# Performance work log

Measured on AMD Instinct MI355X. Metric: run time of the kernel, lower is better.

## Reference

```python
import jax, jax.numpy as jnp
import numpy as np


def setup_inputs() -> dict:
    key = jax.random.key(0)
    k1, k2 = jax.random.split(key)
    B, C, H, W = 8, 32, 384, 384
    # probability-map-like predictions in [0, 1)
    pred = jax.random.uniform(k1, (B, C, H, W), dtype=jnp.float32)
    target = jax.random.randint(k2, (B, H, W), 0, C)  # int labels, all classes present w.h.p.
    return {"pred": pred, "target": target}


def reference(pred, target):
    """J-statistic loss (arXiv:1910.09783). reduction='none', weights=ones.

    Original computes, for each ci != ck:
      loss[b,ci,ck] = w[ci,ck] * log(0.5 + sum_hw pred[b,ci]*(phi[b,ci]-phi[b,ck])/2)
    where phi = one_hot(target)/n_i. The O(C^2) loop collapses to a single
    batched contraction S[b,i,k] = <pred[b,i], phi[b,k]> over spatial dims.
    """
    B, C, H, W = pred.shape
    t1h = jax.nn.one_hot(target, C, dtype=pred.dtype)          # (B,H,W,C)
    t1h = jnp.moveaxis(t1h, -1, 1)                             # (B,C,H,W)
    n_i = t1h.sum(axis=(-2, -1))[:, :, None, None]             # (B,C,1,1) class pixel counts
    phi = t1h / n_i                                            # normalized one-hot
    # S[b,i,k] = sum_hw pred[b,i]*phi[b,k]
    S = jnp.einsum('bihw,bkhw->bik', pred, phi)                # (B,C,C)
    diag = jnp.diagonal(S, axis1=1, axis2=2)                   # (B,C) = S[b,i,i]
    delta_sum = (diag[:, :, None] - S) * 0.5                   # sum_hw pred_i * (phi_i - phi_k)/2
    weights = jnp.ones((C, C), dtype=pred.dtype)
    loss = weights * jnp.log(0.5 + delta_sum)                  # (B,C,C)
    off_diag = 1.0 - jnp.eye(C, dtype=pred.dtype)              # skip ci == ck terms
    j = -(loss * off_diag).sum(axis=(-2, -1))                  # (B,)
    return j
```

## Files before the change

### kernel.cpp

```cpp
#include <hip/hip_runtime.h>


#define BB 8
#define CC 32
#define HW 147456
#define CHUNK_PX 1024
#define NCHUNK (HW / CHUNK_PX)
#define HIST_BPB 16
#define HIST_SEG (HW / HIST_BPB)

typedef __attribute__((ext_vector_type(8))) short short8;
typedef __attribute__((ext_vector_type(4))) float float4v;

__device__ __forceinline__ short bf16_rne(float f) {
    union { float f; unsigned u; } v; v.f = f;
    unsigned u = v.u;
    u += 0x7FFFu + ((u >> 16) & 1u);
    return (short)(u >> 16);
}

__global__ __launch_bounds__(256) void jloss_mfma(
    const float* __restrict__ pred,
    const int*   __restrict__ target,
    float*       __restrict__ T)
{
    const int tid  = threadIdx.x;
    const int w    = tid >> 6;
    const int l    = tid & 63;
    const int quad = l >> 4;
    const int m    = l & 15;
    const int blk  = blockIdx.x;
    const int b    = blk / NCHUNK;
    const int chunk= blk % NCHUNK;

    const long pb_wave = (long)chunk * CHUNK_PX + w * 256;
    const float* predb = pred + (long)b * CC * HW;
    const int*   tgtb  = target + (long)b * HW;

    float4v acc00 = {0,0,0,0}, acc01 = {0,0,0,0};
    float4v acc10 = {0,0,0,0}, acc11 = {0,0,0,0};
    const short one = (short)0x3F80;

    #pragma unroll
    for (int ks = 0; ks < 8; ++ks) {
        const long po = pb_wave + ks * 32 + quad * 8;
        const float* p0 = predb + (long)m * HW + po;
        const float* p1 = p0 + (long)16 * HW;
        const float4 a0l = *(const float4*)p0;
        const float4 a0h = *(const float4*)(p0 + 4);
        const float4 a1l = *(const float4*)p1;
        const float4 a1h = *(const float4*)(p1 + 4);
        const int4 t0 = *(const int4*)(tgtb + po);
        const int4 t1 = *(const int4*)(tgtb + po + 4);

        short8 A0, A1, B0, B1;
        A0[0]=bf16_rne(a0l.x); A0[1]=bf16_rne(a0l.y); A0[2]=bf16_rne(a0l.z); A0[3]=bf16_rne(a0l.w);
        A0[4]=bf16_rne(a0h.x); A0[5]=bf16_rne(a0h.y); A0[6]=bf16_rne(a0h.z); A0[7]=bf16_rne(a0h.w);
        A1[0]=bf16_rne(a1l.x); A1[1]=bf16_rne(a1l.y); A1[2]=bf16_rne(a1l.z); A1[3]=bf16_rne(a1l.w);
        A1[4]=bf16_rne(a1h.x); A1[5]=bf16_rne(a1h.y); A1[6]=bf16_rne(a1h.z); A1[7]=bf16_rne(a1h.w);
        B0[0]=(t0.x==m)?one:(short)0; B0[1]=(t0.y==m)?one:(short)0;
        B0[2]=(t0.z==m)?one:(short)0; B0[3]=(t0.w==m)?one:(short)0;
        B0[4]=(t1.x==m)?one:(short)0; B0[5]=(t1.y==m)?one:(short)0;
        B0[6]=(t1.z==m)?one:(short)0; B0[7]=(t1.w==m)?one:(short)0;
        const int m16 = m + 16;
        B1[0]=(t0.x==m16)?one:(short)0; B1[1]=(t0.y==m16)?one:(short)0;
        B1[2]=(t0.z==m16)?one:(short)0; B1[3]=(t0.w==m16)?one:(short)0;
        B1[4]=(t1.x==m16)?one:(short)0; B1[5]=(t1.y==m16)?one:(short)0;
        B1[6]=(t1.z==m16)?one:(short)0; B1[7]=(t1.w==m16)?one:(short)0;

        acc00 = __builtin_amdgcn_mfma_f32_16x16x32_bf16(A0, B0, acc00, 0, 0, 0);
        acc01 = __builtin_amdgcn_mfma_f32_16x16x32_bf16(A0, B1, acc01, 0, 0, 0);
        acc10 = __builtin_amdgcn_mfma_f32_16x16x32_bf16(A1, B0, acc10, 0, 0, 0);
        acc11 = __builtin_amdgcn_mfma_f32_16x16x32_bf16(A1, B1, acc11, 0, 0, 0);
    }

    __shared__ float red[4][CC][CC];
    #pragma unroll
    for (int r = 0; r < 4; ++r) {
        red[w][quad*4 + r     ][m     ] = acc00[r];
        red[w][quad*4 + r     ][m + 16] = acc01[r];
        red[w][quad*4 + r + 16][m     ] = acc10[r];
        red[w][quad*4 + r + 16][m + 16] = acc11[r];
    }
    __syncthreads();

    float* Tb = T + (long)b * CC * CC;
    const float* rp = &red[0][0][0];
    for (int j = tid; j < CC * CC; j += 256) {
        const float s = rp[j] + rp[1024 + j] + rp[2048 + j] + rp[3072 + j];
        atomicAdd(&Tb[j], s);
    }
}

__global__ __launch_bounds__(256) void jloss_cnt(
    const int* __restrict__ target,
    float*     __restrict__ cnt)
{
    const int tid = threadIdx.x;
    const int w = tid >> 6, l = tid & 63;
    const int blk = blockIdx.x;
    const int b   = blk / HIST_BPB;
    const int seg = blk % HIST_BPB;
    const int* tb = target + (long)b * HW + (long)seg * HIST_SEG + w * (HIST_SEG / 4);

    int c[CC];
    #pragma unroll
    for (int k = 0; k < CC; ++k) c[k] = 0;
    for (int it = 0; it < HIST_SEG / 4 / 64; ++it) {
        const int t = tb[it * 64 + l];
        #pragma unroll
        for (int k = 0; k < CC; ++k)
            c[k] += (int)__popcll(__ballot(t == k));
    }
    if (l == 0) {
        #pragma unroll
        for (int k = 0; k < CC; ++k)
            atomicAdd(&cnt[b * CC + k], (float)c[k]);
    }
}

__global__ __launch_bounds__(256) void jloss_final(
    const float* __restrict__ T,
    const float* __restrict__ cnt,
    float*       __restrict__ out)
{
    const int b   = blockIdx.x;
    const int tid = threadIdx.x;
    __shared__ float diag_s[CC];
    __shared__ float inv_n[CC];
    __shared__ float wsum[4];

    const float* Tb = T + (long)b * CC * CC;
    const float* cb = cnt + b * CC;

    if (tid < CC) {
        const float inv = 1.0f / cb[tid];
        inv_n[tid]  = inv;
        diag_s[tid] = Tb[tid * CC + tid] * inv;
    }
    __syncthreads();

    float sum = 0.0f;
    for (int idx = tid; idx < CC * CC; idx += 256) {
        const int i = idx >> 5;
        const int k = idx & 31;
        if (i != k) {
            const float S = Tb[idx] * inv_n[k];
            sum += logf(0.5f + 0.5f * (diag_s[i] - S));
        }
    }
    #pragma unroll
    for (int off = 32; off > 0; off >>= 1) sum += __shfl_down(sum, off, 64);
    if ((tid & 63) == 0) wsum[tid >> 6] = sum;
    __syncthreads();
    if (tid == 0) out[b] = -(wsum[0] + wsum[1] + wsum[2] + wsum[3]);
}

extern "C" void kernel_launch(void* const* d_in, const int* in_sizes, int n_in,
                              void* d_out, int out_size, void* d_ws, size_t ws_size,
                              hipStream_t stream) {
    const float* pred   = (const float*)d_in[0];
    const int*   target = (const int*)d_in[1];
    float* out = (float*)d_out;

    float* T   = (float*)d_ws;
    float* cnt = (float*)d_ws + BB * CC * CC;

    hipMemsetAsync(d_ws, 0, (BB * CC * CC + BB * CC) * sizeof(float), stream);

    jloss_cnt <<<BB * HIST_BPB, 256, 0, stream>>>(target, cnt);
    jloss_mfma<<<BB * NCHUNK,   256, 0, stream>>>(pred, target, T);
    jloss_final<<<BB, 256, 0, stream>>>(T, cnt, out);
}
```

Before: 268.4 us.

## Fuse class counting into MFMA kernel and cheapen bf16/one-hot packing

Removes the separate histogram kernel. Class pixel counts are now produced inside the MFMA kernel by multiplying a row of bf16 ones against the one-hot B operands, then reduced through shared memory and added atomically into the count buffer. The per-element round-to-nearest bf16 conversion is replaced by a byte-permute that packs two truncated bf16 values per instruction. One-hot operands are built two at a time as packed 32-bit words. It also adds a launch-bounds occupancy hint and limits unrolling to 2, trading VALU work and one kernel launch for two extra MFMAs per step and slightly less accurate (truncated) bf16 inputs.

```diff
diff --git a/kernel.cpp b/kernel.cpp
--- a/kernel.cpp
+++ b/kernel.cpp
@@ -6,23 +6,23 @@
 #define HW 147456
 #define CHUNK_PX 1024
 #define NCHUNK (HW / CHUNK_PX)
-#define HIST_BPB 16
-#define HIST_SEG (HW / HIST_BPB)
 
 typedef __attribute__((ext_vector_type(8))) short short8;
 typedef __attribute__((ext_vector_type(4))) float float4v;
+typedef __attribute__((ext_vector_type(4))) unsigned uint4v;
 
-__device__ __forceinline__ short bf16_rne(float f) {
-    union { float f; unsigned u; } v; v.f = f;
-    unsigned u = v.u;
-    u += 0x7FFFu + ((u >> 16) & 1u);
-    return (short)(u >> 16);
+__device__ __forceinline__ unsigned pk(float lo, float hi) {
+    return __builtin_amdgcn_perm(__float_as_uint(hi), __float_as_uint(lo), 0x07060302u);
+}
+__device__ __forceinline__ unsigned oh2(int ta, int tb, int m) {
+    return (ta == m ? 0x3F80u : 0u) | (tb == m ? 0x3F800000u : 0u);
 }
 
-__global__ __launch_bounds__(256) void jloss_mfma(
+__global__ __launch_bounds__(256, 4) void jloss_mfma(
     const float* __restrict__ pred,
     const int*   __restrict__ target,
-    float*       __restrict__ T)
+    float*       __restrict__ T,
+    float*       __restrict__ cnt)
 {
     const int tid  = threadIdx.x;
     const int w    = tid >> 6;
@@ -39,9 +39,10 @@
 
     float4v acc00 = {0,0,0,0}, acc01 = {0,0,0,0};
     float4v acc10 = {0,0,0,0}, acc11 = {0,0,0,0};
-    const short one = (short)0x3F80;
+    float4v accc0 = {0,0,0,0}, accc1 = {0,0,0,0};
+    const short8 ONES = {0x3F80,0x3F80,0x3F80,0x3F80,0x3F80,0x3F80,0x3F80,0x3F80};
 
-    #pragma unroll
+    #pragma unroll 2
     for (int ks = 0; ks < 8; ++ks) {
         const long po = pb_wave + ks * 32 + quad * 8;
         const float* p0 = predb + (long)m * HW + po;
@@ -53,34 +54,37 @@
         const int4 t0 = *(const int4*)(tgtb + po);
         const int4 t1 = *(const int4*)(tgtb + po + 4);
 
-        short8 A0, A1, B0, B1;
-        A0[0]=bf16_rne(a0l.x); A0[1]=bf16_rne(a0l.y); A0[2]=bf16_rne(a0l.z); A0[3]=bf16_rne(a0l.w);
-        A0[4]=bf16_rne(a0h.x); A0[5]=bf16_rne(a0h.y); A0[6]=bf16_rne(a0h.z); A0[7]=bf16_rne(a0h.w);
-        A1[0]=bf16_rne(a1l.x); A1[1]=bf16_rne(a1l.y); A1[2]=bf16_rne(a1l.z); A1[3]=bf16_rne(a1l.w);
-        A1[4]=bf16_rne(a1h.x); A1[5]=bf16_rne(a1h.y); A1[6]=bf16_rne(a1h.z); A1[7]=bf16_rne(a1h.w);
-        B0[0]=(t0.x==m)?one:(short)0; B0[1]=(t0.y==m)?one:(short)0;
-        B0[2]=(t0.z==m)?one:(short)0; B0[3]=(t0.w==m)?one:(short)0;
-        B0[4]=(t1.x==m)?one:(short)0; B0[5]=(t1.y==m)?one:(short)0;
-        B0[6]=(t1.z==m)?one:(short)0; B0[7]=(t1.w==m)?one:(short)0;
+        union { short8 s; uint4v u; } A0, A1, B0, B1;
+        A0.u[0] = pk(a0l.x, a0l.y); A0.u[1] = pk(a0l.z, a0l.w);
+        A0.u[2] = pk(a0h.x, a0h.y); A0.u[3] = pk(a0h.z, a0h.w);
+        A1.u[0] = pk(a1l.x, a1l.y); A1.u[1] = pk(a1l.z, a1l.w);
+        A1.u[2] = pk(a1h.x, a1h.y); A1.u[3] = pk(a1h.z, a1h.w);
+        B0.u[0] = oh2(t0.x, t0.y, m);      B0.u[1] = oh2(t0.z, t0.w, m);
+        B0.u[2] = oh2(t1.x, t1.y, m);      B0.u[3] = oh2(t1.z, t1.w, m);
         const int m16 = m + 16;
-        B1[0]=(t0.x==m16)?one:(short)0; B1[1]=(t0.y==m16)?one:(short)0;
-        B1[2]=(t0.z==m16)?one:(short)0; B1[3]=(t0.w==m16)?one:(short)0;
-        B1[4]=(t1.x==m16)?one:(short)0; B1[5]=(t1.y==m16)?one:(short)0;
-        B1[6]=(t1.z==m16)?one:(short)0; B1[7]=(t1.w==m16)?one:(short)0;
+        B1.u[0] = oh2(t0.x, t0.y, m16);    B1.u[1] = oh2(t0.z, t0.w, m16);
+        B1.u[2] = oh2(t1.x, t1.y, m16);    B1.u[3] = oh2(t1.z, t1.w, m16);
 
-        acc00 = __builtin_amdgcn_mfma_f32_16x16x32_bf16(A0, B0, acc00, 0, 0, 0);
-        acc01 = __builtin_amdgcn_mfma_f32_16x16x32_bf16(A0, B1, acc01, 0, 0, 0);
-        acc10 = __builtin_amdgcn_mfma_f32_16x16x32_bf16(A1, B0, acc10, 0, 0, 0);
-        acc11 = __builtin_amdgcn_mfma_f32_16x16x32_bf16(A1, B1, acc11, 0, 0, 0);
+        acc00 = __builtin_amdgcn_mfma_f32_16x16x32_bf16(A0.s, B0.s, acc00, 0, 0, 0);
+        acc01 = __builtin_amdgcn_mfma_f32_16x16x32_bf16(A0.s, B1.s, acc01, 0, 0, 0);
+        acc10 = __builtin_amdgcn_mfma_f32_16x16x32_bf16(A1.s, B0.s, acc10, 0, 0, 0);
+        acc11 = __builtin_amdgcn_mfma_f32_16x16x32_bf16(A1.s, B1.s, acc11, 0, 0, 0);
+        accc0 = __builtin_amdgcn_mfma_f32_16x16x32_bf16(ONES, B0.s, accc0, 0, 0, 0);
+        accc1 = __builtin_amdgcn_mfma_f32_16x16x32_bf16(ONES, B1.s, accc1, 0, 0, 0);
     }
 
     __shared__ float red[4][CC][CC];
+    __shared__ float redc[4][CC];
     #pragma unroll
     for (int r = 0; r < 4; ++r) {
         red[w][quad*4 + r     ][m     ] = acc00[r];
         red[w][quad*4 + r     ][m + 16] = acc01[r];
         red[w][quad*4 + r + 16][m     ] = acc10[r];
         red[w][quad*4 + r + 16][m + 16] = acc11[r];
+    }
+    if (quad == 0) {
+        redc[w][m]      = accc0[0];
+        redc[w][m + 16] = accc1[0];
     }
     __syncthreads();
 
@@ -90,33 +94,9 @@
         const float s = rp[j] + rp[1024 + j] + rp[2048 + j] + rp[3072 + j];
         atomicAdd(&Tb[j], s);
     }
-}
-
-__global__ __launch_bounds__(256) void jloss_cnt(
-    const int* __restrict__ target,
-    float*     __restrict__ cnt)
-{
-    const int tid = threadIdx.x;
-    const int w = tid >> 6, l = tid & 63;
-    const int blk = blockIdx.x;
-    const int b   = blk / HIST_BPB;
-    const int seg = blk % HIST_BPB;
-    const int* tb = target + (long)b * HW + (long)seg * HIST_SEG + w * (HIST_SEG / 4);
-
-    int c[CC];
-    #pragma unroll
-    for (int k = 0; k < CC; ++k) c[k] = 0;
-    for (int it = 0; it < HIST_SEG / 4 / 64; ++it) {
-        const int t = tb[it * 64 + l];
-        #pragma unroll
-        for (int k = 0; k < CC; ++k)
-            c[k] += (int)__popcll(__ballot(t == k));
-    }
-    if (l == 0) {
-        #pragma unroll
-        for (int k = 0; k < CC; ++k)
-            atomicAdd(&cnt[b * CC + k], (float)c[k]);
-    }
+    if (tid < CC)
+        atomicAdd(&cnt[b * CC + tid],
+                  redc[0][tid] + redc[1][tid] + redc[2][tid] + redc[3][tid]);
 }
 
 __global__ __launch_bounds__(256) void jloss_final(
@@ -168,7 +148,6 @@
 
     hipMemsetAsync(d_ws, 0, (BB * CC * CC + BB * CC) * sizeof(float), stream);
 
-    jloss_cnt <<<BB * HIST_BPB, 256, 0, stream>>>(target, cnt);
-    jloss_mfma<<<BB * NCHUNK,   256, 0, stream>>>(pred, target, T);
+    jloss_mfma <<<BB * NCHUNK, 256, 0, stream>>>(pred, target, T, cnt);
     jloss_final<<<BB, 256, 0, stream>>>(T, cnt, out);
 }
```

New measurement: 222.5 us. 1.21x faster.
